# Kernel optimization log

Hardware: AMD Instinct MI355X
Metric: run time of the kernel (lower is better)

Reference implementation:

```python
import jax, jax.numpy as jnp
import numpy as np

B = 262144      # batch
DIN = 100       # input covariate dim (cfg_density[0][0])
H = 64          # hidden dim
G = 10          # num_grid -> density output dim G+1
NH = 5          # number of dosage-bucket heads in Multi_head


def setup_inputs() -> dict:
    key = jax.random.key(0)
    ks = jax.random.split(key, 16)
    s = 0.05
    return {
        "dosage": jax.random.uniform(ks[0], (B,), dtype=jnp.float32),
        "x": jax.random.normal(ks[1], (B, DIN), dtype=jnp.float32),
        # density feature MLP (two Linear+ReLU layers)
        "dW0": jax.random.normal(ks[2], (DIN, H), dtype=jnp.float32) * s,
        "db0": jax.random.normal(ks[3], (H,), dtype=jnp.float32) * s,
        "dW1": jax.random.normal(ks[4], (H, H), dtype=jnp.float32) * s,
        "db1": jax.random.normal(ks[5], (H,), dtype=jnp.float32) * s,
        # Density_Block: Linear(H -> G+1) then softmax + grid interpolation
        "dbW": jax.random.normal(ks[6], (H, G + 1), dtype=jnp.float32) * s,
        "dbB": jax.random.normal(ks[7], (G + 1,), dtype=jnp.float32) * s,
        # Multi_head: 5 structurally identical heads, params stacked on axis 0
        # layer0: Treat_Linear(64 -> 64, relu, istreat=1)
        "W0": jax.random.normal(ks[8], (NH, H, H), dtype=jnp.float32) * s,
        "tw0": jax.random.normal(ks[9], (NH, H), dtype=jnp.float32) * s,
        "b0": jax.random.normal(ks[10], (NH, H), dtype=jnp.float32) * s,
        # layer1 (last): Treat_Linear(64 -> 1, no act, istreat=1)
        "W1": jax.random.normal(ks[11], (NH, H, 1), dtype=jnp.float32) * s,
        "tw1": jax.random.normal(ks[12], (NH, 1), dtype=jnp.float32) * s,
        "b1": jax.random.normal(ks[13], (NH, 1), dtype=jnp.float32) * s,
    }


def reference(dosage, x, dW0, db0, dW1, db1, dbW, dbB, W0, tw0, b0, W1, tw1, b1):
    # hidden feature MLP
    hidden = jax.nn.relu(x @ dW0 + db0)
    hidden = jax.nn.relu(hidden @ dW1 + db1)            # [B, H]

    # ---- Density_Block: softmax over grid, dual gather + linear interpolation
    p = jax.nn.softmax(hidden @ dbW + dbB, axis=1)      # [B, G+1]
    tB = dosage * G
    U = jnp.ceil(tB)
    inter = 1.0 - (U - tB)                              # fractional position in cell
    Ui = U.astype(jnp.int32)
    Li = Ui - 1
    Li = Li + (Li < 0).astype(jnp.int32)                # clamp L=-1 -> 0
    pL = jnp.take_along_axis(p, Li[:, None], axis=1)[:, 0]
    pU = jnp.take_along_axis(p, Ui[:, None], axis=1)[:, 0]
    g = pL + (pU - pL) * inter                          # [B]

    # ---- Multi_head: 5 heads on dosage buckets [0,.2),[.2,.4),...,[.8,1.)
    t = dosage
    # layer0: out = feat @ W + t * tw + b, relu; compute all heads, select later
    h0 = jax.nn.relu(
        jnp.einsum('bi,hio->bho', hidden, W0)
        + t[:, None, None] * tw0[None]
        + b0[None]
    )                                                   # [B, NH, H]
    # last layer: no activation
    out1 = (jnp.einsum('bho,hoj->bhj', h0, W1)
            + t[:, None, None] * tw1[None]
            + b1[None])                                 # [B, NH, 1]
    bucket = jnp.clip(jnp.floor(t * NH).astype(jnp.int32), 0, NH - 1)
    Q = jnp.take_along_axis(out1, bucket[:, None, None], axis=1)[:, 0, :]  # [B, 1]
    return g, Q
```

## Files before the change

### kernel.cpp

```cpp
#include <hip/hip_runtime.h>

typedef __attribute__((ext_vector_type(8))) short  short8;
typedef __attribute__((ext_vector_type(4))) float  floatx4;

constexpr int DIN = 100;
constexpr int H   = 64;
constexpr int G   = 10;
constexpr int NH  = 5;
constexpr int MWG = 128;
constexpr int HPITCH = H + 1;

constexpr int NF_DW0 = 16, NF_DW1 = 8, NF_DBW = 2, NF_W0 = 40;
constexpr int NF_LDS = NF_DW0 + NF_DW1 + NF_DBW;
constexpr int NF_TOT = NF_LDS + NF_W0;

__device__ __forceinline__ unsigned short f2bf(float f) {
    union { float f; unsigned u; } v{f};
    unsigned r = v.u + 0x7FFF + ((v.u >> 16) & 1);
    return (unsigned short)(r >> 16);
}

__global__ __launch_bounds__(64) void pack_kernel(
    const float* __restrict__ dW0, const float* __restrict__ dW1,
    const float* __restrict__ dbW, const float* __restrict__ W0,
    unsigned short* __restrict__ ws)
{
    const int f = blockIdx.x;
    const int lane = threadIdx.x;
    const int q = lane >> 4, cl = lane & 15;
    float v[8];
    if (f < NF_DW0) {
        int c = f >> 2, g = f & 3;
        #pragma unroll
        for (int j = 0; j < 8; ++j) {
            int k = c * 32 + q * 8 + j, n = g * 16 + cl;
            v[j] = (k < DIN) ? dW0[k * H + n] : 0.0f;
        }
    } else if (f < NF_DW0 + NF_DW1) {
        int r = f - NF_DW0; int c = r >> 2, g = r & 3;
        #pragma unroll
        for (int j = 0; j < 8; ++j) {
            int k = c * 32 + q * 8 + j, n = g * 16 + cl;
            v[j] = dW1[k * H + n];
        }
    } else if (f < NF_LDS) {
        int c = f - (NF_DW0 + NF_DW1);
        #pragma unroll
        for (int j = 0; j < 8; ++j) {
            int k = c * 32 + q * 8 + j, n = cl;
            v[j] = (n <= G) ? dbW[k * (G + 1) + n] : 0.0f;
        }
    } else {
        int r = f - NF_LDS; int h = r >> 3; r &= 7; int c = r >> 2, g = r & 3;
        #pragma unroll
        for (int j = 0; j < 8; ++j) {
            int k = c * 32 + q * 8 + j, n = g * 16 + cl;
            v[j] = W0[(h * H + k) * H + n];
        }
    }
    short8 s;
    #pragma unroll
    for (int j = 0; j < 8; ++j) s[j] = (short)f2bf(v[j]);
    *(short8*)(ws + (size_t)(f * 64 + lane) * 8) = s;
}

__global__ __launch_bounds__(256) void drnet_mfma(
    const float* __restrict__ dosage, const float* __restrict__ x,
    const float* __restrict__ db0, const float* __restrict__ db1,
    const float* __restrict__ dbB,
    const float* __restrict__ tw0, const float* __restrict__ b0,
    const float* __restrict__ W1, const float* __restrict__ tw1,
    const float* __restrict__ b1,
    const unsigned short* __restrict__ wsfrag,
    float* __restrict__ outg, float* __restrict__ outq)
{
    __shared__ float  hbuf[MWG * HPITCH];
    __shared__ short8 wlds[NF_LDS * 64];
    __shared__ float  tbuf[MWG];

    const int tid  = threadIdx.x;
    const int wave = tid >> 6, lane = tid & 63;
    const int q = lane >> 4, cl = lane & 15;
    const int rowbase = blockIdx.x * MWG;
    const int wrow = wave * 32;

    {
        const floatx4* src = (const floatx4*)wsfrag;
        floatx4* dst = (floatx4*)wlds;
        #pragma unroll
        for (int i = tid; i < NF_LDS * 64; i += 256) dst[i] = src[i];
    }
    if (tid < MWG) tbuf[tid] = dosage[rowbase + tid];
    __syncthreads();

    float t8[2][4];
    #pragma unroll
    for (int mt = 0; mt < 2; ++mt)
        #pragma unroll
        for (int r = 0; r < 4; ++r) t8[mt][r] = tbuf[wrow + mt * 16 + 4 * q + r];

    floatx4 acc[2][4];

    #pragma unroll
    for (int mt = 0; mt < 2; ++mt)
        #pragma unroll
        for (int g = 0; g < 4; ++g) acc[mt][g] = (floatx4)0.0f;

    #pragma unroll
    for (int cch = 0; cch < 4; ++cch) {
        short8 a[2];
        #pragma unroll
        for (int mt = 0; mt < 2; ++mt) {
            const float* xr = x + (size_t)(rowbase + wrow + mt * 16 + cl) * DIN;
            float f[8];
            if (cch < 3) {
                floatx4 u0 = *(const floatx4*)(xr + cch * 32 + q * 8);
                floatx4 u1 = *(const floatx4*)(xr + cch * 32 + q * 8 + 4);
                f[0]=u0.x; f[1]=u0.y; f[2]=u0.z; f[3]=u0.w;
                f[4]=u1.x; f[5]=u1.y; f[6]=u1.z; f[7]=u1.w;
            } else {
                if (q == 0) {
                    floatx4 u0 = *(const floatx4*)(xr + 96);
                    f[0]=u0.x; f[1]=u0.y; f[2]=u0.z; f[3]=u0.w;
                    f[4]=f[5]=f[6]=f[7]=0.0f;
                } else {
                    #pragma unroll
                    for (int j = 0; j < 8; ++j) f[j] = 0.0f;
                }
            }
            short8 s;
            #pragma unroll
            for (int j = 0; j < 8; ++j) s[j] = (short)f2bf(f[j]);
            a[mt] = s;
        }
        #pragma unroll
        for (int g = 0; g < 4; ++g) {
            short8 bf = wlds[(cch * 4 + g) * 64 + lane];
            #pragma unroll
            for (int mt = 0; mt < 2; ++mt)
                acc[mt][g] = __builtin_amdgcn_mfma_f32_16x16x32_bf16(a[mt], bf, acc[mt][g], 0, 0, 0);
        }
    }
    #pragma unroll
    for (int g = 0; g < 4; ++g) {
        float bias = db0[g * 16 + cl];
        #pragma unroll
        for (int mt = 0; mt < 2; ++mt)
            #pragma unroll
            for (int r = 0; r < 4; ++r)
                hbuf[(wrow + mt * 16 + 4 * q + r) * HPITCH + g * 16 + cl] =
                    fmaxf(acc[mt][g][r] + bias, 0.0f);
    }

    #pragma unroll
    for (int mt = 0; mt < 2; ++mt)
        #pragma unroll
        for (int g = 0; g < 4; ++g) acc[mt][g] = (floatx4)0.0f;

    #pragma unroll
    for (int cch = 0; cch < 2; ++cch) {
        short8 a[2];
        #pragma unroll
        for (int mt = 0; mt < 2; ++mt) {
            const float* hr = hbuf + (wrow + mt * 16 + cl) * HPITCH + cch * 32 + q * 8;
            short8 s;
            #pragma unroll
            for (int j = 0; j < 8; ++j) s[j] = (short)f2bf(hr[j]);
            a[mt] = s;
        }
        #pragma unroll
        for (int g = 0; g < 4; ++g) {
            short8 bf = wlds[(NF_DW0 + cch * 4 + g) * 64 + lane];
            #pragma unroll
            for (int mt = 0; mt < 2; ++mt)
                acc[mt][g] = __builtin_amdgcn_mfma_f32_16x16x32_bf16(a[mt], bf, acc[mt][g], 0, 0, 0);
        }
    }
    #pragma unroll
    for (int g = 0; g < 4; ++g) {
        float bias = db1[g * 16 + cl];
        #pragma unroll
        for (int mt = 0; mt < 2; ++mt)
            #pragma unroll
            for (int r = 0; r < 4; ++r)
                hbuf[(wrow + mt * 16 + 4 * q + r) * HPITCH + g * 16 + cl] =
                    fmaxf(acc[mt][g][r] + bias, 0.0f);
    }

    short8 af[2][2];
    #pragma unroll
    for (int mt = 0; mt < 2; ++mt)
        #pragma unroll
        for (int cch = 0; cch < 2; ++cch) {
            const float* hr = hbuf + (wrow + mt * 16 + cl) * HPITCH + cch * 32 + q * 8;
            short8 s;
            #pragma unroll
            for (int j = 0; j < 8; ++j) s[j] = (short)f2bf(hr[j]);
            af[mt][cch] = s;
        }

    floatx4 accd[2];
    accd[0] = (floatx4)0.0f; accd[1] = (floatx4)0.0f;
    #pragma unroll
    for (int cch = 0; cch < 2; ++cch) {
        short8 bf = wlds[(NF_DW0 + NF_DW1 + cch) * 64 + lane];
        #pragma unroll
        for (int mt = 0; mt < 2; ++mt)
            accd[mt] = __builtin_amdgcn_mfma_f32_16x16x32_bf16(af[mt][cch], bf, accd[mt], 0, 0, 0);
    }
    const float dbBv = (cl <= G) ? dbB[cl] : 0.0f;
    float gout[2][4];
    #pragma unroll
    for (int mt = 0; mt < 2; ++mt)
        #pragma unroll
        for (int r = 0; r < 4; ++r) {
            float l = (cl <= G) ? (accd[mt][r] + dbBv) : -1e30f;
            float m = l;
            m = fmaxf(m, __shfl_xor(m, 1)); m = fmaxf(m, __shfl_xor(m, 2));
            m = fmaxf(m, __shfl_xor(m, 4)); m = fmaxf(m, __shfl_xor(m, 8));
            float e = __expf(l - m);
            float s = e;
            s += __shfl_xor(s, 1); s += __shfl_xor(s, 2);
            s += __shfl_xor(s, 4); s += __shfl_xor(s, 8);
            const float t  = t8[mt][r];
            const float tB = t * (float)G;
            const float U  = ceilf(tB);
            const float inter = 1.0f - (U - tB);
            int Ui = (int)U; int Li = Ui - 1; if (Li < 0) Li = 0;
            float pL = __shfl(e, q * 16 + Li);
            float pU = __shfl(e, q * 16 + Ui);
            gout[mt][r] = (pL + (pU - pL) * inter) / s;
        }
    if (cl == 0) {
        #pragma unroll
        for (int mt = 0; mt < 2; ++mt) {
            floatx4 gv = { gout[mt][0], gout[mt][1], gout[mt][2], gout[mt][3] };
            *(floatx4*)(outg + rowbase + wrow + mt * 16 + 4 * q) = gv;
        }
    }

    float qacc[2][4] = {{0,0,0,0},{0,0,0,0}};
    int   bk8[2][4];
    #pragma unroll
    for (int mt = 0; mt < 2; ++mt)
        #pragma unroll
        for (int r = 0; r < 4; ++r) {
            int bk = (int)floorf(t8[mt][r] * (float)NH);
            bk8[mt][r] = min(max(bk, 0), NH - 1);
        }

    #pragma unroll 1
    for (int h = 0; h < NH; ++h) {
        floatx4 acch[2][4];
        #pragma unroll
        for (int mt = 0; mt < 2; ++mt)
            #pragma unroll
            for (int g = 0; g < 4; ++g) acch[mt][g] = (floatx4)0.0f;
        #pragma unroll
        for (int cch = 0; cch < 2; ++cch) {
            #pragma unroll
            for (int g = 0; g < 4; ++g) {
                short8 bf = *(const short8*)(wsfrag +
                    (size_t)((NF_LDS + h * 8 + cch * 4 + g) * 64 + lane) * 8);
                #pragma unroll
                for (int mt = 0; mt < 2; ++mt)
                    acch[mt][g] = __builtin_amdgcn_mfma_f32_16x16x32_bf16(af[mt][cch], bf, acch[mt][g], 0, 0, 0);
            }
        }
        #pragma unroll
        for (int g = 0; g < 4; ++g) {
            const float tw0v = tw0[h * H + g * 16 + cl];
            const float b0v  = b0 [h * H + g * 16 + cl];
            const float w1v  = W1 [h * H + g * 16 + cl];
            #pragma unroll
            for (int mt = 0; mt < 2; ++mt)
                #pragma unroll
                for (int r = 0; r < 4; ++r) {
                    float h0 = acch[mt][g][r] + t8[mt][r] * tw0v + b0v;
                    float c  = fmaxf(h0, 0.0f) * w1v;
                    qacc[mt][r] += (bk8[mt][r] == h) ? c : 0.0f;
                }
        }
    }
    float qv[2][4];
    #pragma unroll
    for (int mt = 0; mt < 2; ++mt)
        #pragma unroll
        for (int r = 0; r < 4; ++r) {
            float s = qacc[mt][r];
            s += __shfl_xor(s, 1); s += __shfl_xor(s, 2);
            s += __shfl_xor(s, 4); s += __shfl_xor(s, 8);
            const int h = bk8[mt][r];
            qv[mt][r] = s + t8[mt][r] * tw1[h] + b1[h];
        }
    if (cl == 0) {
        #pragma unroll
        for (int mt = 0; mt < 2; ++mt) {
            floatx4 Qv = { qv[mt][0], qv[mt][1], qv[mt][2], qv[mt][3] };
            *(floatx4*)(outq + rowbase + wrow + mt * 16 + 4 * q) = Qv;
        }
    }
}

extern "C" void kernel_launch(void* const* d_in, const int* in_sizes, int n_in,
                              void* d_out, int out_size, void* d_ws, size_t ws_size,
                              hipStream_t stream) {
    const float* dosage = (const float*)d_in[0];
    const float* x      = (const float*)d_in[1];
    const float* dW0    = (const float*)d_in[2];
    const float* db0    = (const float*)d_in[3];
    const float* dW1    = (const float*)d_in[4];
    const float* db1    = (const float*)d_in[5];
    const float* dbW    = (const float*)d_in[6];
    const float* dbB    = (const float*)d_in[7];
    const float* W0     = (const float*)d_in[8];
    const float* tw0    = (const float*)d_in[9];
    const float* b0     = (const float*)d_in[10];
    const float* W1     = (const float*)d_in[11];
    const float* tw1    = (const float*)d_in[12];
    const float* b1     = (const float*)d_in[13];

    const int Btot = in_sizes[0];
    float* outg = (float*)d_out;
    float* outq = outg + Btot;
    unsigned short* ws = (unsigned short*)d_ws;

    pack_kernel<<<NF_TOT, 64, 0, stream>>>(dW0, dW1, dbW, W0, ws);
    drnet_mfma<<<Btot / MWG, 256, 0, stream>>>(dosage, x, db0, db1, dbB,
                                               tw0, b0, W1, tw1, b1,
                                               ws, outg, outq);
}
```

Baseline: 227.4 us.

## Drop LDS weight staging, store hidden as bf16, defer per-head epilogue

```diff
diff --git a/kernel.cpp b/kernel.cpp
--- a/kernel.cpp
+++ b/kernel.cpp
@@ -2,22 +2,44 @@
 
 typedef __attribute__((ext_vector_type(8))) short  short8;
 typedef __attribute__((ext_vector_type(4))) float  floatx4;
+typedef __attribute__((ext_vector_type(4))) int    intx4;
 
 constexpr int DIN = 100;
 constexpr int H   = 64;
 constexpr int G   = 10;
 constexpr int NH  = 5;
 constexpr int MWG = 128;
-constexpr int HPITCH = H + 1;
-
-constexpr int NF_DW0 = 16, NF_DW1 = 8, NF_DBW = 2, NF_W0 = 40;
-constexpr int NF_LDS = NF_DW0 + NF_DW1 + NF_DBW;
-constexpr int NF_TOT = NF_LDS + NF_W0;
-
-__device__ __forceinline__ unsigned short f2bf(float f) {
+constexpr int HP  = 72;
+
+constexpr int NF_DW0 = 16, NF_DW1 = 8, NF_DBW = 2;
+constexpr int NF_LIN = NF_DW0 + NF_DW1 + NF_DBW;
+constexpr int NF_TOT = NF_LIN + 40;
+
+__device__ __forceinline__ unsigned short f2bf_rne(float f) {
     union { float f; unsigned u; } v{f};
     unsigned r = v.u + 0x7FFF + ((v.u >> 16) & 1);
     return (unsigned short)(r >> 16);
+}
+
+__device__ __forceinline__ short8 pack8(const float* f) {
+    intx4 p;
+    #pragma unroll
+    for (int j = 0; j < 4; ++j) {
+        unsigned a = __float_as_uint(f[2 * j])     + 0x8000u;
+        unsigned b = __float_as_uint(f[2 * j + 1]) + 0x8000u;
+        p[j] = (int)((b & 0xFFFF0000u) | (a >> 16));
+    }
+    union { intx4 i; short8 s; } u; u.i = p;
+    return u.s;
+}
+
+__device__ __forceinline__ unsigned short f2bf_hu(float f) {
+    return (unsigned short)((__float_as_uint(f) + 0x8000u) >> 16);
+}
+
+__device__ __forceinline__ short8 ldfrag(const unsigned short* __restrict__ ws,
+                                         int f, int lane) {
+    return *(const short8*)(ws + (size_t)(f * 64 + lane) * 8);
 }
 
 __global__ __launch_bounds__(64) void pack_kernel(
@@ -43,7 +65,7 @@
             int k = c * 32 + q * 8 + j, n = g * 16 + cl;
             v[j] = dW1[k * H + n];
         }
-    } else if (f < NF_LDS) {
+    } else if (f < NF_LIN) {
         int c = f - (NF_DW0 + NF_DW1);
         #pragma unroll
         for (int j = 0; j < 8; ++j) {
@@ -51,7 +73,7 @@
             v[j] = (n <= G) ? dbW[k * (G + 1) + n] : 0.0f;
         }
     } else {
-        int r = f - NF_LDS; int h = r >> 3; r &= 7; int c = r >> 2, g = r & 3;
+        int r = f - NF_LIN; int h = r >> 3; r &= 7; int c = r >> 2, g = r & 3;
         #pragma unroll
         for (int j = 0; j < 8; ++j) {
             int k = c * 32 + q * 8 + j, n = g * 16 + cl;
@@ -60,7 +82,7 @@
     }
     short8 s;
     #pragma unroll
-    for (int j = 0; j < 8; ++j) s[j] = (short)f2bf(v[j]);
+    for (int j = 0; j < 8; ++j) s[j] = (short)f2bf_rne(v[j]);
     *(short8*)(ws + (size_t)(f * 64 + lane) * 8) = s;
 }
 
@@ -74,44 +96,33 @@
     const unsigned short* __restrict__ wsfrag,
     float* __restrict__ outg, float* __restrict__ outq)
 {
-    __shared__ float  hbuf[MWG * HPITCH];
-    __shared__ short8 wlds[NF_LDS * 64];
-    __shared__ float  tbuf[MWG];
-
+    __shared__ unsigned short hbuf[MWG * HP];
     const int tid  = threadIdx.x;
     const int wave = tid >> 6, lane = tid & 63;
     const int q = lane >> 4, cl = lane & 15;
-    const int rowbase = blockIdx.x * MWG;
-    const int wrow = wave * 32;
-
-    {
-        const floatx4* src = (const floatx4*)wsfrag;
-        floatx4* dst = (floatx4*)wlds;
-        #pragma unroll
-        for (int i = tid; i < NF_LDS * 64; i += 256) dst[i] = src[i];
-    }
-    if (tid < MWG) tbuf[tid] = dosage[rowbase + tid];
-    __syncthreads();
+    const int rowbase = blockIdx.x * MWG + wave * 32;
+    unsigned short* hb = hbuf + wave * 32 * HP;
 
     float t8[2][4];
-    #pragma unroll
-    for (int mt = 0; mt < 2; ++mt)
-        #pragma unroll
-        for (int r = 0; r < 4; ++r) t8[mt][r] = tbuf[wrow + mt * 16 + 4 * q + r];
+    int   bk8[2][4];
+    #pragma unroll
+    for (int mt = 0; mt < 2; ++mt)
+        #pragma unroll
+        for (int r = 0; r < 4; ++r) {
+            float t = dosage[rowbase + mt * 16 + 4 * q + r];
+            t8[mt][r] = t;
+            int bk = (int)floorf(t * (float)NH);
+            bk8[mt][r] = min(max(bk, 0), NH - 1);
+        }
 
     floatx4 acc[2][4];
 
-    #pragma unroll
-    for (int mt = 0; mt < 2; ++mt)
-        #pragma unroll
-        for (int g = 0; g < 4; ++g) acc[mt][g] = (floatx4)0.0f;
-
-    #pragma unroll
-    for (int cch = 0; cch < 4; ++cch) {
-        short8 a[2];
-        #pragma unroll
-        for (int mt = 0; mt < 2; ++mt) {
-            const float* xr = x + (size_t)(rowbase + wrow + mt * 16 + cl) * DIN;
+    short8 a1[2][4];
+    #pragma unroll
+    for (int mt = 0; mt < 2; ++mt) {
+        const float* xr = x + (size_t)(rowbase + mt * 16 + cl) * DIN;
+        #pragma unroll
+        for (int cch = 0; cch < 4; ++cch) {
             float f[8];
             if (cch < 3) {
                 floatx4 u0 = *(const floatx4*)(xr + cch * 32 + q * 8);
@@ -128,19 +139,22 @@
                     for (int j = 0; j < 8; ++j) f[j] = 0.0f;
                 }
             }
-            short8 s;
-            #pragma unroll
-            for (int j = 0; j < 8; ++j) s[j] = (short)f2bf(f[j]);
-            a[mt] = s;
-        }
+            a1[mt][cch] = pack8(f);
+        }
+    }
+    #pragma unroll
+    for (int mt = 0; mt < 2; ++mt)
+        #pragma unroll
+        for (int g = 0; g < 4; ++g) acc[mt][g] = (floatx4)0.0f;
+    #pragma unroll
+    for (int cch = 0; cch < 4; ++cch)
         #pragma unroll
         for (int g = 0; g < 4; ++g) {
-            short8 bf = wlds[(cch * 4 + g) * 64 + lane];
+            short8 bf = ldfrag(wsfrag, cch * 4 + g, lane);
             #pragma unroll
             for (int mt = 0; mt < 2; ++mt)
-                acc[mt][g] = __builtin_amdgcn_mfma_f32_16x16x32_bf16(a[mt], bf, acc[mt][g], 0, 0, 0);
-        }
-    }
+                acc[mt][g] = __builtin_amdgcn_mfma_f32_16x16x32_bf16(a1[mt][cch], bf, acc[mt][g], 0, 0, 0);
+        }
     #pragma unroll
     for (int g = 0; g < 4; ++g) {
         float bias = db0[g * 16 + cl];
@@ -148,34 +162,29 @@
         for (int mt = 0; mt < 2; ++mt)
             #pragma unroll
             for (int r = 0; r < 4; ++r)
-                hbuf[(wrow + mt * 16 + 4 * q + r) * HPITCH + g * 16 + cl] =
-                    fmaxf(acc[mt][g][r] + bias, 0.0f);
-    }
-
+                hb[(mt * 16 + 4 * q + r) * HP + g * 16 + cl] =
+                    f2bf_hu(fmaxf(acc[mt][g][r] + bias, 0.0f));
+    }
+
+    short8 a2[2][2];
+    #pragma unroll
+    for (int mt = 0; mt < 2; ++mt)
+        #pragma unroll
+        for (int cch = 0; cch < 2; ++cch)
+            a2[mt][cch] = *(const short8*)(hb + (mt * 16 + cl) * HP + cch * 32 + q * 8);
     #pragma unroll
     for (int mt = 0; mt < 2; ++mt)
         #pragma unroll
         for (int g = 0; g < 4; ++g) acc[mt][g] = (floatx4)0.0f;
-
-    #pragma unroll
-    for (int cch = 0; cch < 2; ++cch) {
-        short8 a[2];
-        #pragma unroll
-        for (int mt = 0; mt < 2; ++mt) {
-            const float* hr = hbuf + (wrow + mt * 16 + cl) * HPITCH + cch * 32 + q * 8;
-            short8 s;
-            #pragma unroll
-            for (int j = 0; j < 8; ++j) s[j] = (short)f2bf(hr[j]);
-            a[mt] = s;
-        }
+    #pragma unroll
+    for (int cch = 0; cch < 2; ++cch)
         #pragma unroll
         for (int g = 0; g < 4; ++g) {
-            short8 bf = wlds[(NF_DW0 + cch * 4 + g) * 64 + lane];
+            short8 bf = ldfrag(wsfrag, NF_DW0 + cch * 4 + g, lane);
             #pragma unroll
             for (int mt = 0; mt < 2; ++mt)
-                acc[mt][g] = __builtin_amdgcn_mfma_f32_16x16x32_bf16(a[mt], bf, acc[mt][g], 0, 0, 0);
-        }
-    }
+                acc[mt][g] = __builtin_amdgcn_mfma_f32_16x16x32_bf16(a2[mt][cch], bf, acc[mt][g], 0, 0, 0);
+        }
     #pragma unroll
     for (int g = 0; g < 4; ++g) {
         float bias = db1[g * 16 + cl];
@@ -183,27 +192,22 @@
         for (int mt = 0; mt < 2; ++mt)
             #pragma unroll
             for (int r = 0; r < 4; ++r)
-                hbuf[(wrow + mt * 16 + 4 * q + r) * HPITCH + g * 16 + cl] =
-                    fmaxf(acc[mt][g][r] + bias, 0.0f);
+                hb[(mt * 16 + 4 * q + r) * HP + g * 16 + cl] =
+                    f2bf_hu(fmaxf(acc[mt][g][r] + bias, 0.0f));
     }
 
     short8 af[2][2];
     #pragma unroll
     for (int mt = 0; mt < 2; ++mt)
         #pragma unroll
-        for (int cch = 0; cch < 2; ++cch) {
-            const float* hr = hbuf + (wrow + mt * 16 + cl) * HPITCH + cch * 32 + q * 8;
-            short8 s;
-            #pragma unroll
-            for (int j = 0; j < 8; ++j) s[j] = (short)f2bf(hr[j]);
-            af[mt][cch] = s;
-        }
+        for (int cch = 0; cch < 2; ++cch)
+            af[mt][cch] = *(const short8*)(hb + (mt * 16 + cl) * HP + cch * 32 + q * 8);
 
     floatx4 accd[2];
     accd[0] = (floatx4)0.0f; accd[1] = (floatx4)0.0f;
     #pragma unroll
     for (int cch = 0; cch < 2; ++cch) {
-        short8 bf = wlds[(NF_DW0 + NF_DW1 + cch) * 64 + lane];
+        short8 bf = ldfrag(wsfrag, NF_DW0 + NF_DW1 + cch, lane);
         #pragma unroll
         for (int mt = 0; mt < 2; ++mt)
             accd[mt] = __builtin_amdgcn_mfma_f32_16x16x32_bf16(af[mt][cch], bf, accd[mt], 0, 0, 0);
@@ -235,19 +239,17 @@
         #pragma unroll
         for (int mt = 0; mt < 2; ++mt) {
             floatx4 gv = { gout[mt][0], gout[mt][1], gout[mt][2], gout[mt][3] };
-            *(floatx4*)(outg + rowbase + wrow + mt * 16 + 4 * q) = gv;
-        }
-    }
-
-    float qacc[2][4] = {{0,0,0,0},{0,0,0,0}};
-    int   bk8[2][4];
-    #pragma unroll
-    for (int mt = 0; mt < 2; ++mt)
-        #pragma unroll
-        for (int r = 0; r < 4; ++r) {
-            int bk = (int)floorf(t8[mt][r] * (float)NH);
-            bk8[mt][r] = min(max(bk, 0), NH - 1);
-        }
+            *(floatx4*)(outg + rowbase + mt * 16 + 4 * q) = gv;
+        }
+    }
+
+    float asel[2][4][4];
+    #pragma unroll
+    for (int mt = 0; mt < 2; ++mt)
+        #pragma unroll
+        for (int g = 0; g < 4; ++g)
+            #pragma unroll
+            for (int r = 0; r < 4; ++r) asel[mt][g][r] = 0.0f;
 
     #pragma unroll 1
     for (int h = 0; h < NH; ++h) {
@@ -257,47 +259,53 @@
             #pragma unroll
             for (int g = 0; g < 4; ++g) acch[mt][g] = (floatx4)0.0f;
         #pragma unroll
-        for (int cch = 0; cch < 2; ++cch) {
+        for (int cch = 0; cch < 2; ++cch)
             #pragma unroll
             for (int g = 0; g < 4; ++g) {
-                short8 bf = *(const short8*)(wsfrag +
-                    (size_t)((NF_LDS + h * 8 + cch * 4 + g) * 64 + lane) * 8);
+                short8 bf = ldfrag(wsfrag, NF_LIN + h * 8 + cch * 4 + g, lane);
                 #pragma unroll
                 for (int mt = 0; mt < 2; ++mt)
                     acch[mt][g] = __builtin_amdgcn_mfma_f32_16x16x32_bf16(af[mt][cch], bf, acch[mt][g], 0, 0, 0);
             }
-        }
-        #pragma unroll
-        for (int g = 0; g < 4; ++g) {
-            const float tw0v = tw0[h * H + g * 16 + cl];
-            const float b0v  = b0 [h * H + g * 16 + cl];
-            const float w1v  = W1 [h * H + g * 16 + cl];
-            #pragma unroll
-            for (int mt = 0; mt < 2; ++mt)
+        #pragma unroll
+        for (int mt = 0; mt < 2; ++mt)
+            #pragma unroll
+            for (int r = 0; r < 4; ++r) {
+                bool sel = (bk8[mt][r] == h);
                 #pragma unroll
-                for (int r = 0; r < 4; ++r) {
-                    float h0 = acch[mt][g][r] + t8[mt][r] * tw0v + b0v;
-                    float c  = fmaxf(h0, 0.0f) * w1v;
-                    qacc[mt][r] += (bk8[mt][r] == h) ? c : 0.0f;
-                }
-        }
-    }
-    float qv[2][4];
+                for (int g = 0; g < 4; ++g)
+                    asel[mt][g][r] = sel ? acch[mt][g][r] : asel[mt][g][r];
+            }
+    }
+
+    float qp[2][4] = {{0,0,0,0},{0,0,0,0}};
+    #pragma unroll
+    for (int g = 0; g < 4; ++g) {
+        const int ci = g * 16 + cl;
+        #pragma unroll
+        for (int mt = 0; mt < 2; ++mt)
+            #pragma unroll
+            for (int r = 0; r < 4; ++r) {
+                const int off = bk8[mt][r] * H + ci;
+                float h0 = asel[mt][g][r] + t8[mt][r] * tw0[off] + b0[off];
+                qp[mt][r] += fmaxf(h0, 0.0f) * W1[off];
+            }
+    }
     #pragma unroll
     for (int mt = 0; mt < 2; ++mt)
         #pragma unroll
         for (int r = 0; r < 4; ++r) {
-            float s = qacc[mt][r];
+            float s = qp[mt][r];
             s += __shfl_xor(s, 1); s += __shfl_xor(s, 2);
             s += __shfl_xor(s, 4); s += __shfl_xor(s, 8);
             const int h = bk8[mt][r];
-            qv[mt][r] = s + t8[mt][r] * tw1[h] + b1[h];
+            qp[mt][r] = s + t8[mt][r] * tw1[h] + b1[h];
         }
     if (cl == 0) {
         #pragma unroll
         for (int mt = 0; mt < 2; ++mt) {
-            floatx4 Qv = { qv[mt][0], qv[mt][1], qv[mt][2], qv[mt][3] };
-            *(floatx4*)(outq + rowbase + wrow + mt * 16 + 4 * q) = Qv;
+            floatx4 Qv = { qp[mt][0], qp[mt][1], qp[mt][2], qp[mt][3] };
+            *(floatx4*)(outq + rowbase + mt * 16 + 4 * q) = Qv;
         }
     }
 }
```

Result: no change. 229.4 us (+0.9%).
